# Kernel optimization log

Measured on AMD Instinct MI355X. Metric: run time of the kernel, lower is better.

Reference implementation:

```python
import jax, jax.numpy as jnp
import numpy as np

N, FIN, HID, HEADS, DHEAD = 4096, 512, 256, 4, 256
TOPK = 29  # hard-coded t=29 in HAN1.forward
FOUT = HEADS * DHEAD  # 1024


def setup_inputs() -> dict:
    key = jax.random.key(0)
    ks = jax.random.split(key, 12)
    h = jax.random.normal(ks[0], (N, FIN), dtype=jnp.float32)
    simlar = jax.random.normal(ks[1], (N, N), dtype=jnp.float32)
    # binary adjacency, avg degree ~41 so top-k (29) actually prunes
    adj = (jax.random.uniform(ks[2], (N, N)) < 0.01).astype(jnp.float32)
    s = 0.05
    W_trans = jax.random.normal(ks[3], (FIN, HID), dtype=jnp.float32) * s
    gat_W = jax.random.normal(ks[4], (HID, FOUT), dtype=jnp.float32) * s
    attn_l = jax.random.normal(ks[5], (HEADS, DHEAD), dtype=jnp.float32) * s
    attn_r = jax.random.normal(ks[6], (HEADS, DHEAD), dtype=jnp.float32) * s
    gat_bias = jnp.zeros((FOUT,), dtype=jnp.float32)
    sem_W1 = jax.random.normal(ks[7], (FOUT, 128), dtype=jnp.float32) * s
    sem_b1 = jnp.zeros((128,), dtype=jnp.float32)
    sem_W2 = jax.random.normal(ks[8], (128, 1), dtype=jnp.float32) * s
    return {"h": h, "simlar": simlar, "adj": adj, "W_trans": W_trans,
            "gat_W": gat_W, "attn_l": attn_l, "attn_r": attn_r,
            "gat_bias": gat_bias, "sem_W1": sem_W1, "sem_b1": sem_b1,
            "sem_W2": sem_W2}


def reference(h, simlar, adj, W_trans, gat_W, attn_l, attn_r, gat_bias,
              sem_W1, sem_b1, sem_W2):
    lrelu01 = lambda x: jax.nn.leaky_relu(x, 0.01)  # nn.LeakyReLU default
    # ---- adjacency sparsification: per-row top-k of filtered similarity ----
    filt = lrelu01(adj * simlar) * (adj > 0).astype(adj.dtype)  # [N,N]
    top_vals, top_idx = jax.lax.top_k(filt, TOPK)               # [N,TOPK]
    rows = jnp.arange(N)[:, None]
    newmat = jnp.zeros_like(filt).at[rows, top_idx].set(top_vals)
    mask = newmat != 0  # mask[src, dst]: edge src->dst (nonzero() semantics)
    # ---- feature transform (dropout p=0 -> identity) ----
    x = lrelu01(h @ W_trans)                                    # [N,HID]
    # ---- GATConv (DGL semantics, negative_slope=0.2, activation=elu) ----
    feat = (x @ gat_W).reshape(N, HEADS, DHEAD)                 # [N,H,D]
    el = jnp.einsum('nhd,hd->nh', feat, attn_l)                 # src scores
    er = jnp.einsum('nhd,hd->nh', feat, attn_r)                 # dst scores
    e = jax.nn.leaky_relu(el[:, None, :] + er[None, :, :], 0.2) # [src,dst,H]
    mask3 = mask[:, :, None]
    e = jnp.where(mask3, e, jnp.asarray(-1e30, e.dtype))
    emax = jnp.max(e, axis=0, keepdims=True)
    exp_e = jnp.where(mask3, jnp.exp(e - emax), 0.0)
    denom = jnp.sum(exp_e, axis=0, keepdims=True)
    alpha = exp_e / jnp.maximum(denom, 1e-20)  # zero-in-degree -> zero output
    rst = jnp.einsum('sdh,shf->dhf', alpha, feat)               # [N,H,D]
    rst = jax.nn.elu(rst + gat_bias.reshape(HEADS, DHEAD))
    sem = rst.reshape(N, FOUT)                                  # flatten(1)
    # ---- semantic attention over meta-paths (here: 1 meta-path) ----
    z = sem[:, None, :]                                         # [N,1,F]
    w = (jnp.tanh(z @ sem_W1 + sem_b1) @ sem_W2).mean(0)        # [1,1]
    beta = jax.nn.softmax(w, axis=0)                            # [1,1]
    out = (beta[None, :, :] * z).sum(1)                         # [N,F]
    return out
```

## Files before the change

kernel.cpp:

```cpp
#include <hip/hip_runtime.h>
#include <hip/hip_bf16.h>
#include <math.h>

#define N 4096
#define FIN 512
#define HID 256
#define HEADS 4
#define DHEAD 256
#define FOUT 1024
#define TOPK 29
#define CAP 64
#define CAPC 96

typedef __attribute__((ext_vector_type(8))) short short8;
typedef __attribute__((ext_vector_type(4))) float f32x4;
typedef __hip_bfloat16 bf16;

__device__ __forceinline__ float bflo(unsigned int u) {
  return __uint_as_float(u << 16);
}
__device__ __forceinline__ float bfhi(unsigned int u) {
  return __uint_as_float(u & 0xffff0000u);
}

__global__ __launch_bounds__(256) void scan_kernel(
    const float* __restrict__ h, const float* __restrict__ W_trans,
    const float* __restrict__ gat_W, const float* __restrict__ adj,
    const float* __restrict__ simlar, bf16* __restrict__ hb,
    bf16* __restrict__ Wtb, bf16* __restrict__ gWtb,
    int* __restrict__ colcnt, int* __restrict__ colsrc) {
  const int t = threadIdx.x;
  const int s = blockIdx.x;
  {
    const int H4 = N * FIN / 4;
    const int WT = HID * FIN;
    const int GT = FOUT * HID;
    const int total = H4 + WT + GT;
    const int stride = gridDim.x * 256;
    for (int i = s * 256 + t; i < total; i += stride) {
      if (i < H4) {
        const float4 v = reinterpret_cast<const float4*>(h)[i];
        bf16 tmp[4];
        tmp[0] = __float2bfloat16(v.x);
        tmp[1] = __float2bfloat16(v.y);
        tmp[2] = __float2bfloat16(v.z);
        tmp[3] = __float2bfloat16(v.w);
        *reinterpret_cast<ushort4*>(&hb[(size_t)i * 4]) =
            *reinterpret_cast<ushort4*>(tmp);
      } else if (i < H4 + WT) {
        const int j = i - H4;
        const int row = j >> 9, k = j & 511;
        Wtb[j] = __float2bfloat16(W_trans[(size_t)k * HID + row]);
      } else {
        const int j = i - H4 - WT;
        const int row = j >> 8, k = j & 255;
        gWtb[j] = __float2bfloat16(gat_W[(size_t)k * FOUT + row]);
      }
    }
  }
  __shared__ float swv[CAP];
  __shared__ int swi[CAP];
  __shared__ int cnt;
  if (t == 0) cnt = 0;
  __syncthreads();
  const float4* rowadj = reinterpret_cast<const float4*>(adj) + (size_t)s * (N / 4);
  const float4* rowsim = reinterpret_cast<const float4*>(simlar) + (size_t)s * (N / 4);
  float4 a[4];
#pragma unroll
  for (int it = 0; it < 4; ++it) a[it] = rowadj[it * 256 + t];
#pragma unroll
  for (int it = 0; it < 4; ++it) {
    const int j = it * 256 + t;
    if (a[it].x > 0.f || a[it].y > 0.f || a[it].z > 0.f || a[it].w > 0.f) {
      const float4 s4 = rowsim[j];
      const float aa[4] = {a[it].x, a[it].y, a[it].z, a[it].w};
      const float ss[4] = {s4.x, s4.y, s4.z, s4.w};
#pragma unroll
      for (int c = 0; c < 4; ++c) {
        if (aa[c] > 0.f && ss[c] > 0.f) {
          const int p = atomicAdd(&cnt, 1);
          if (p < CAP) {
            swv[p] = ss[c];
            swi[p] = j * 4 + c;
          }
        }
      }
    }
  }
  __syncthreads();
  const int C = min(cnt, CAP);
  if (t < C) {
    const float x = swv[t];
    int rk = 0;
    for (int jj = 0; jj < C; ++jj) rk += (swv[jj] > x);
    if (rk < TOPK) {
      const int d = swi[t];
      const int p = atomicAdd(&colcnt[d], 1);
      if (p < CAPC) colsrc[(size_t)d * CAPC + p] = s;
    }
  }
}

template <int OUTMODE>
__global__ __launch_bounds__(256) void gemm_mfma(const bf16* __restrict__ A,
                                                 const bf16* __restrict__ Bt,
                                                 bf16* __restrict__ Cb,
                                                 int M, int Nn, int K) {
  __shared__ bf16 As[64][72];
  __shared__ bf16 Bs[64][72];
  const int t = threadIdx.x;
  const int bm = blockIdx.x * 64, bn = blockIdx.y * 64;
  const int w = t >> 6, lane = t & 63, r = lane & 15, g = lane >> 4;
  const int m = t >> 2, c0 = (t & 3) * 8;
  f32x4 acc[4] = {};
  for (int k0 = 0; k0 < K; k0 += 64) {
    const bf16* arow = &A[(size_t)(bm + m) * K + k0];
    const bf16* brow = &Bt[(size_t)(bn + m) * K + k0];
    *reinterpret_cast<int4*>(&As[m][c0]) = *reinterpret_cast<const int4*>(&arow[c0]);
    *reinterpret_cast<int4*>(&As[m][c0 + 32]) = *reinterpret_cast<const int4*>(&arow[c0 + 32]);
    *reinterpret_cast<int4*>(&Bs[m][c0]) = *reinterpret_cast<const int4*>(&brow[c0]);
    *reinterpret_cast<int4*>(&Bs[m][c0 + 32]) = *reinterpret_cast<const int4*>(&brow[c0 + 32]);
    __syncthreads();
    const short8 a0 = *reinterpret_cast<short8*>(&As[w * 16 + r][g * 8]);
    const short8 a1 = *reinterpret_cast<short8*>(&As[w * 16 + r][32 + g * 8]);
#pragma unroll
    for (int j = 0; j < 4; ++j) {
      const short8 b0 = *reinterpret_cast<short8*>(&Bs[j * 16 + r][g * 8]);
      const short8 b1 = *reinterpret_cast<short8*>(&Bs[j * 16 + r][32 + g * 8]);
      acc[j] = __builtin_amdgcn_mfma_f32_16x16x32_bf16(a0, b0, acc[j], 0, 0, 0);
      acc[j] = __builtin_amdgcn_mfma_f32_16x16x32_bf16(a1, b1, acc[j], 0, 0, 0);
    }
    __syncthreads();
  }
#pragma unroll
  for (int j = 0; j < 4; ++j)
#pragma unroll
    for (int q = 0; q < 4; ++q) {
      const int row = bm + w * 16 + g * 4 + q;
      const int col = bn + j * 16 + r;
      float v = acc[j][q];
      if (OUTMODE == 1) v = v >= 0.f ? v : 0.01f * v;
      Cb[(size_t)row * Nn + col] = __float2bfloat16(v);
    }
}

__global__ __launch_bounds__(256) void elr_kernel(const bf16* __restrict__ featb,
                                                  const float* __restrict__ attn_l,
                                                  const float* __restrict__ attn_r,
                                                  float* __restrict__ el,
                                                  float* __restrict__ er) {
  const int n = blockIdx.x;
  const int h = threadIdx.x >> 6, lane = threadIdx.x & 63;
  const uint2 v2 = *reinterpret_cast<const uint2*>(
      &featb[(size_t)n * FOUT + h * DHEAD + lane * 4]);
  const float f0 = bflo(v2.x), f1 = bfhi(v2.x), f2 = bflo(v2.y), f3 = bfhi(v2.y);
  const float4 al = *reinterpret_cast<const float4*>(&attn_l[h * DHEAD + lane * 4]);
  const float4 ar = *reinterpret_cast<const float4*>(&attn_r[h * DHEAD + lane * 4]);
  float sl = f0 * al.x + f1 * al.y + f2 * al.z + f3 * al.w;
  float sr = f0 * ar.x + f1 * ar.y + f2 * ar.z + f3 * ar.w;
  for (int off = 32; off; off >>= 1) {
    sl += __shfl_xor(sl, off);
    sr += __shfl_xor(sr, off);
  }
  if (lane == 0) {
    el[n * HEADS + h] = sl;
    er[n * HEADS + h] = sr;
  }
}

__global__ __launch_bounds__(256) void agg_kernel(const int* __restrict__ colcnt,
                                                  const int* __restrict__ colsrc,
                                                  const float* __restrict__ el,
                                                  const float* __restrict__ er,
                                                  const bf16* __restrict__ featb,
                                                  const float* __restrict__ bias,
                                                  float* __restrict__ out) {
  __shared__ int tmp[2][CAPC];
  __shared__ int slist[2][CAPC];
  __shared__ float pbuf[2][HEADS][CAPC];
  const int t = threadIdx.x;
  const int grp = t >> 7;
  const int g = t & 127;
  const int d = blockIdx.x * 2 + grp;
  const int C = min(colcnt[d], CAPC);
  if (g < C) tmp[grp][g] = colsrc[(size_t)d * CAPC + g];
  __syncthreads();
  if (g < C) {
    const int v = tmp[grp][g];
    int rk = 0;
    for (int j = 0; j < C; ++j) rk += (tmp[grp][j] < v);
    slist[grp][rk] = v;
  }
  __syncthreads();
  const int h = g >> 5;
  const int hl = g & 31;
  const float er_dh = er[d * HEADS + h];
  float m = -INFINITY;
  for (int i = hl; i < C; i += 32) {
    float e = el[slist[grp][i] * HEADS + h] + er_dh;
    e = e >= 0.f ? e : 0.2f * e;
    pbuf[grp][h][i] = e;
    m = fmaxf(m, e);
  }
#pragma unroll
  for (int off = 16; off; off >>= 1) m = fmaxf(m, __shfl_xor(m, off));
  float dsum = 0.f;
  for (int i = hl; i < C; i += 32) {
    const float p = __expf(pbuf[grp][h][i] - m);
    pbuf[grp][h][i] = p;
    dsum += p;
  }
#pragma unroll
  for (int off = 16; off; off >>= 1) dsum += __shfl_xor(dsum, off);
  __syncthreads();
  float acc[8] = {};
  int i = 0;
  for (; i + 2 <= C; i += 2) {
    const float p0 = pbuf[grp][h][i];
    const float p1 = pbuf[grp][h][i + 1];
    const uint4 v0 = *reinterpret_cast<const uint4*>(
        &featb[(size_t)slist[grp][i] * FOUT + g * 8]);
    const uint4 v1 = *reinterpret_cast<const uint4*>(
        &featb[(size_t)slist[grp][i + 1] * FOUT + g * 8]);
    acc[0] = fmaf(p0, bflo(v0.x), acc[0]);
    acc[1] = fmaf(p0, bfhi(v0.x), acc[1]);
    acc[2] = fmaf(p0, bflo(v0.y), acc[2]);
    acc[3] = fmaf(p0, bfhi(v0.y), acc[3]);
    acc[4] = fmaf(p0, bflo(v0.z), acc[4]);
    acc[5] = fmaf(p0, bfhi(v0.z), acc[5]);
    acc[6] = fmaf(p0, bflo(v0.w), acc[6]);
    acc[7] = fmaf(p0, bfhi(v0.w), acc[7]);
    acc[0] = fmaf(p1, bflo(v1.x), acc[0]);
    acc[1] = fmaf(p1, bfhi(v1.x), acc[1]);
    acc[2] = fmaf(p1, bflo(v1.y), acc[2]);
    acc[3] = fmaf(p1, bfhi(v1.y), acc[3]);
    acc[4] = fmaf(p1, bflo(v1.z), acc[4]);
    acc[5] = fmaf(p1, bfhi(v1.z), acc[5]);
    acc[6] = fmaf(p1, bflo(v1.w), acc[6]);
    acc[7] = fmaf(p1, bfhi(v1.w), acc[7]);
  }
  if (i < C) {
    const float p0 = pbuf[grp][h][i];
    const uint4 v0 = *reinterpret_cast<const uint4*>(
        &featb[(size_t)slist[grp][i] * FOUT + g * 8]);
    acc[0] = fmaf(p0, bflo(v0.x), acc[0]);
    acc[1] = fmaf(p0, bfhi(v0.x), acc[1]);
    acc[2] = fmaf(p0, bflo(v0.y), acc[2]);
    acc[3] = fmaf(p0, bfhi(v0.y), acc[3]);
    acc[4] = fmaf(p0, bflo(v0.z), acc[4]);
    acc[5] = fmaf(p0, bfhi(v0.z), acc[5]);
    acc[6] = fmaf(p0, bflo(v0.w), acc[6]);
    acc[7] = fmaf(p0, bfhi(v0.w), acc[7]);
  }
  const float inv = C > 0 ? 1.f / dsum : 0.f;
  float o[8];
#pragma unroll
  for (int k = 0; k < 8; ++k) {
    const float r = acc[k] * inv + bias[g * 8 + k];
    o[k] = r > 0.f ? r : expm1f(r);
  }
  float* op = &out[(size_t)d * FOUT + g * 8];
  *reinterpret_cast<float4*>(op) = make_float4(o[0], o[1], o[2], o[3]);
  *reinterpret_cast<float4*>(op + 4) = make_float4(o[4], o[5], o[6], o[7]);
}

extern "C" void kernel_launch(void* const* d_in, const int* in_sizes, int n_in,
                              void* d_out, int out_size, void* d_ws, size_t ws_size,
                              hipStream_t stream) {
  const float* h        = (const float*)d_in[0];
  const float* simlar   = (const float*)d_in[1];
  const float* adj      = (const float*)d_in[2];
  const float* W_trans  = (const float*)d_in[3];
  const float* gat_W    = (const float*)d_in[4];
  const float* attn_l   = (const float*)d_in[5];
  const float* attn_r   = (const float*)d_in[6];
  const float* gat_bias = (const float*)d_in[7];
  float* out = (float*)d_out;

  char* ws = (char*)d_ws;
  const size_t MB = 1 << 20;
  bf16* hb    = (bf16*)(ws);
  bf16* Wtb   = (bf16*)(ws + 4 * MB);
  bf16* gWtb  = (bf16*)(ws + 4 * MB + 512 * 1024);
  bf16* xb    = (bf16*)(ws + 5 * MB);
  float* el   = (float*)(ws + 7 * MB);
  float* er   = (float*)(ws + 7 * MB + 65536);
  bf16* featb = (bf16*)(ws + 8 * MB);
  int* colcnt = (int*)(ws + 16 * MB);
  int* colsrc = (int*)(ws + 17 * MB);

  hipMemsetAsync(colcnt, 0, (size_t)N * sizeof(int), stream);
  scan_kernel<<<N, 256, 0, stream>>>(h, W_trans, gat_W, adj, simlar,
                                     hb, Wtb, gWtb, colcnt, colsrc);
  gemm_mfma<1><<<dim3(N / 64, HID / 64), 256, 0, stream>>>(hb, Wtb, xb, N, HID, FIN);
  gemm_mfma<2><<<dim3(N / 64, FOUT / 64), 256, 0, stream>>>(xb, gWtb, featb, N, FOUT, HID);
  elr_kernel<<<N, 256, 0, stream>>>(featb, attn_l, attn_r, el, er);
  agg_kernel<<<N / 2, 256, 0, stream>>>(colcnt, colsrc, el, er, featb, gat_bias, out);
}
```

Measured before the change: 75.59 us.

## Fold attention vectors into weights, add 128-tile GEMM, rebalance aggregation

Precomputes gat_W·attn_l and gat_W·attn_r inside the scan kernel, so el/er come straight from x with a small 256-wide dot product and no longer need to read featb. The feature GEMM moves to a new 128x128 tile kernel with larger per-wave accumulators to improve operand reuse. The aggregation kernel is reorganised so each block handles 4 destinations over half the feature width, one wave per destination. The el/er values now come from fp32 folded weights instead of bf16 feat, which slightly changes rounding, and the 128-tile GEMM launches only 256 blocks.

```diff
diff --git a/kernel.cpp b/kernel.cpp
--- a/kernel.cpp
+++ b/kernel.cpp
@@ -25,17 +25,20 @@
 
 __global__ __launch_bounds__(256) void scan_kernel(
     const float* __restrict__ h, const float* __restrict__ W_trans,
-    const float* __restrict__ gat_W, const float* __restrict__ adj,
+    const float* __restrict__ gat_W, const float* __restrict__ attn_l,
+    const float* __restrict__ attn_r, const float* __restrict__ adj,
     const float* __restrict__ simlar, bf16* __restrict__ hb,
     bf16* __restrict__ Wtb, bf16* __restrict__ gWtb,
-    int* __restrict__ colcnt, int* __restrict__ colsrc) {
+    float* __restrict__ alr2, int* __restrict__ colcnt,
+    int* __restrict__ colsrc) {
   const int t = threadIdx.x;
   const int s = blockIdx.x;
   {
     const int H4 = N * FIN / 4;
     const int WT = HID * FIN;
     const int GT = FOUT * HID;
-    const int total = H4 + WT + GT;
+    const int AL = 2 * HEADS * HID;
+    const int total = H4 + WT + GT + AL;
     const int stride = gridDim.x * 256;
     for (int i = s * 256 + t; i < total; i += stride) {
       if (i < H4) {
@@ -51,10 +54,20 @@
         const int j = i - H4;
         const int row = j >> 9, k = j & 511;
         Wtb[j] = __float2bfloat16(W_trans[(size_t)k * HID + row]);
-      } else {
+      } else if (i < H4 + WT + GT) {
         const int j = i - H4 - WT;
         const int row = j >> 8, k = j & 255;
         gWtb[j] = __float2bfloat16(gat_W[(size_t)k * FOUT + row]);
+      } else {
+        const int j = i - H4 - WT - GT;
+        const float* vec = (j < 1024) ? attn_l : attn_r;
+        const int jj = j & 1023;
+        const int hh = jj >> 8, k = jj & 255;
+        const float* wp = &gat_W[(size_t)k * FOUT + hh * DHEAD];
+        const float* vp = &vec[hh * DHEAD];
+        float acc = 0.f;
+        for (int d = 0; d < DHEAD; ++d) acc = fmaf(wp[d], vp[d], acc);
+        alr2[j] = acc;
       }
     }
   }
@@ -101,11 +114,10 @@
   }
 }
 
-template <int OUTMODE>
-__global__ __launch_bounds__(256) void gemm_mfma(const bf16* __restrict__ A,
-                                                 const bf16* __restrict__ Bt,
-                                                 bf16* __restrict__ Cb,
-                                                 int M, int Nn, int K) {
+__global__ __launch_bounds__(256) void gemm_mfma64(const bf16* __restrict__ A,
+                                                   const bf16* __restrict__ Bt,
+                                                   bf16* __restrict__ Cb,
+                                                   int M, int Nn, int K) {
   __shared__ bf16 As[64][72];
   __shared__ bf16 Bs[64][72];
   const int t = threadIdx.x;
@@ -139,32 +151,86 @@
       const int row = bm + w * 16 + g * 4 + q;
       const int col = bn + j * 16 + r;
       float v = acc[j][q];
-      if (OUTMODE == 1) v = v >= 0.f ? v : 0.01f * v;
+      v = v >= 0.f ? v : 0.01f * v;
       Cb[(size_t)row * Nn + col] = __float2bfloat16(v);
     }
 }
 
-__global__ __launch_bounds__(256) void elr_kernel(const bf16* __restrict__ featb,
-                                                  const float* __restrict__ attn_l,
-                                                  const float* __restrict__ attn_r,
-                                                  float* __restrict__ el,
-                                                  float* __restrict__ er) {
-  const int n = blockIdx.x;
-  const int h = threadIdx.x >> 6, lane = threadIdx.x & 63;
-  const uint2 v2 = *reinterpret_cast<const uint2*>(
-      &featb[(size_t)n * FOUT + h * DHEAD + lane * 4]);
-  const float f0 = bflo(v2.x), f1 = bfhi(v2.x), f2 = bflo(v2.y), f3 = bfhi(v2.y);
-  const float4 al = *reinterpret_cast<const float4*>(&attn_l[h * DHEAD + lane * 4]);
-  const float4 ar = *reinterpret_cast<const float4*>(&attn_r[h * DHEAD + lane * 4]);
-  float sl = f0 * al.x + f1 * al.y + f2 * al.z + f3 * al.w;
-  float sr = f0 * ar.x + f1 * ar.y + f2 * ar.z + f3 * ar.w;
+__global__ __launch_bounds__(256) void gemm_mfma128(const bf16* __restrict__ A,
+                                                    const bf16* __restrict__ Bt,
+                                                    bf16* __restrict__ Cb,
+                                                    int M, int Nn, int K) {
+  __shared__ bf16 As[128][40];
+  __shared__ bf16 Bs[128][40];
+  const int t = threadIdx.x;
+  const int bm = blockIdx.x * 128, bn = blockIdx.y * 128;
+  const int w = t >> 6, lane = t & 63, r = lane & 15, g = lane >> 4;
+  const int m = t >> 1, c0 = (t & 1) * 16;
+  f32x4 acc[2][8] = {};
+  for (int k0 = 0; k0 < K; k0 += 32) {
+    const bf16* arow = &A[(size_t)(bm + m) * K + k0 + c0];
+    const bf16* brow = &Bt[(size_t)(bn + m) * K + k0 + c0];
+    *reinterpret_cast<int4*>(&As[m][c0]) = *reinterpret_cast<const int4*>(arow);
+    *reinterpret_cast<int4*>(&As[m][c0 + 8]) = *reinterpret_cast<const int4*>(arow + 8);
+    *reinterpret_cast<int4*>(&Bs[m][c0]) = *reinterpret_cast<const int4*>(brow);
+    *reinterpret_cast<int4*>(&Bs[m][c0 + 8]) = *reinterpret_cast<const int4*>(brow + 8);
+    __syncthreads();
+    const short8 a0 = *reinterpret_cast<short8*>(&As[w * 32 + r][g * 8]);
+    const short8 a1 = *reinterpret_cast<short8*>(&As[w * 32 + 16 + r][g * 8]);
+#pragma unroll
+    for (int j = 0; j < 8; ++j) {
+      const short8 b = *reinterpret_cast<short8*>(&Bs[j * 16 + r][g * 8]);
+      acc[0][j] = __builtin_amdgcn_mfma_f32_16x16x32_bf16(a0, b, acc[0][j], 0, 0, 0);
+      acc[1][j] = __builtin_amdgcn_mfma_f32_16x16x32_bf16(a1, b, acc[1][j], 0, 0, 0);
+    }
+    __syncthreads();
+  }
+#pragma unroll
+  for (int i = 0; i < 2; ++i)
+#pragma unroll
+    for (int j = 0; j < 8; ++j)
+#pragma unroll
+      for (int q = 0; q < 4; ++q) {
+        const int row = bm + w * 32 + i * 16 + g * 4 + q;
+        const int col = bn + j * 16 + r;
+        Cb[(size_t)row * Nn + col] = __float2bfloat16(acc[i][j][q]);
+      }
+}
+
+__global__ __launch_bounds__(256) void elr2_kernel(const bf16* __restrict__ xb,
+                                                   const float* __restrict__ alr2,
+                                                   float* __restrict__ el,
+                                                   float* __restrict__ er) {
+  __shared__ float alrs[2048];
+  const int t = threadIdx.x;
+  for (int i = t; i < 2048; i += 256) alrs[i] = alr2[i];
+  __syncthreads();
+  const int wv = t >> 6, lane = t & 63;
+  const int n = blockIdx.x * 4 + wv;
+  const uint2 v2 = *reinterpret_cast<const uint2*>(&xb[(size_t)n * HID + lane * 4]);
+  const float xf[4] = {bflo(v2.x), bfhi(v2.x), bflo(v2.y), bfhi(v2.y)};
+  float pl[4], pr[4];
+#pragma unroll
+  for (int hh = 0; hh < 4; ++hh) {
+    const int base = hh * 256 + lane * 4;
+    pl[hh] = xf[0] * alrs[base] + xf[1] * alrs[base + 1] +
+             xf[2] * alrs[base + 2] + xf[3] * alrs[base + 3];
+    pr[hh] = xf[0] * alrs[1024 + base] + xf[1] * alrs[1024 + base + 1] +
+             xf[2] * alrs[1024 + base + 2] + xf[3] * alrs[1024 + base + 3];
+  }
   for (int off = 32; off; off >>= 1) {
-    sl += __shfl_xor(sl, off);
-    sr += __shfl_xor(sr, off);
+#pragma unroll
+    for (int hh = 0; hh < 4; ++hh) {
+      pl[hh] += __shfl_xor(pl[hh], off);
+      pr[hh] += __shfl_xor(pr[hh], off);
+    }
   }
   if (lane == 0) {
-    el[n * HEADS + h] = sl;
-    er[n * HEADS + h] = sr;
+#pragma unroll
+    for (int hh = 0; hh < 4; ++hh) {
+      el[n * HEADS + hh] = pl[hh];
+      er[n * HEADS + hh] = pr[hh];
+    }
   }
 }
 
@@ -175,53 +241,56 @@
                                                   const bf16* __restrict__ featb,
                                                   const float* __restrict__ bias,
                                                   float* __restrict__ out) {
-  __shared__ int tmp[2][CAPC];
-  __shared__ int slist[2][CAPC];
-  __shared__ float pbuf[2][HEADS][CAPC];
-  const int t = threadIdx.x;
-  const int grp = t >> 7;
-  const int g = t & 127;
-  const int d = blockIdx.x * 2 + grp;
+  __shared__ int tmp[4][CAPC];
+  __shared__ int slist[4][CAPC];
+  __shared__ float pbuf[4][2][CAPC];
+  const int t = threadIdx.x;
+  const int grp = t >> 6;
+  const int lane = t & 63;
+  const int hf = blockIdx.x & 1;
+  const int d = (blockIdx.x >> 1) * 4 + grp;
   const int C = min(colcnt[d], CAPC);
-  if (g < C) tmp[grp][g] = colsrc[(size_t)d * CAPC + g];
-  __syncthreads();
-  if (g < C) {
-    const int v = tmp[grp][g];
+  for (int i = lane; i < C; i += 64) tmp[grp][i] = colsrc[(size_t)d * CAPC + i];
+  __syncthreads();
+  for (int i = lane; i < C; i += 64) {
+    const int v = tmp[grp][i];
     int rk = 0;
     for (int j = 0; j < C; ++j) rk += (tmp[grp][j] < v);
     slist[grp][rk] = v;
   }
   __syncthreads();
-  const int h = g >> 5;
-  const int hl = g & 31;
+  const int sl = lane >> 5;
+  const int h = hf * 2 + sl;
+  const int hl = lane & 31;
   const float er_dh = er[d * HEADS + h];
   float m = -INFINITY;
   for (int i = hl; i < C; i += 32) {
     float e = el[slist[grp][i] * HEADS + h] + er_dh;
     e = e >= 0.f ? e : 0.2f * e;
-    pbuf[grp][h][i] = e;
+    pbuf[grp][sl][i] = e;
     m = fmaxf(m, e);
   }
 #pragma unroll
   for (int off = 16; off; off >>= 1) m = fmaxf(m, __shfl_xor(m, off));
   float dsum = 0.f;
   for (int i = hl; i < C; i += 32) {
-    const float p = __expf(pbuf[grp][h][i] - m);
-    pbuf[grp][h][i] = p;
+    const float p = __expf(pbuf[grp][sl][i] - m);
+    pbuf[grp][sl][i] = p;
     dsum += p;
   }
 #pragma unroll
   for (int off = 16; off; off >>= 1) dsum += __shfl_xor(dsum, off);
   __syncthreads();
+  const size_t dimoff = hf * 512 + lane * 8;
   float acc[8] = {};
   int i = 0;
   for (; i + 2 <= C; i += 2) {
-    const float p0 = pbuf[grp][h][i];
-    const float p1 = pbuf[grp][h][i + 1];
+    const float p0 = pbuf[grp][sl][i];
+    const float p1 = pbuf[grp][sl][i + 1];
     const uint4 v0 = *reinterpret_cast<const uint4*>(
-        &featb[(size_t)slist[grp][i] * FOUT + g * 8]);
+        &featb[(size_t)slist[grp][i] * FOUT + dimoff]);
     const uint4 v1 = *reinterpret_cast<const uint4*>(
-        &featb[(size_t)slist[grp][i + 1] * FOUT + g * 8]);
+        &featb[(size_t)slist[grp][i + 1] * FOUT + dimoff]);
     acc[0] = fmaf(p0, bflo(v0.x), acc[0]);
     acc[1] = fmaf(p0, bfhi(v0.x), acc[1]);
     acc[2] = fmaf(p0, bflo(v0.y), acc[2]);
@@ -240,9 +309,9 @@
     acc[7] = fmaf(p1, bfhi(v1.w), acc[7]);
   }
   if (i < C) {
-    const float p0 = pbuf[grp][h][i];
+    const float p0 = pbuf[grp][sl][i];
     const uint4 v0 = *reinterpret_cast<const uint4*>(
-        &featb[(size_t)slist[grp][i] * FOUT + g * 8]);
+        &featb[(size_t)slist[grp][i] * FOUT + dimoff]);
     acc[0] = fmaf(p0, bflo(v0.x), acc[0]);
     acc[1] = fmaf(p0, bfhi(v0.x), acc[1]);
     acc[2] = fmaf(p0, bflo(v0.y), acc[2]);
@@ -256,10 +325,10 @@
   float o[8];
 #pragma unroll
   for (int k = 0; k < 8; ++k) {
-    const float r = acc[k] * inv + bias[g * 8 + k];
+    const float r = acc[k] * inv + bias[dimoff + k];
     o[k] = r > 0.f ? r : expm1f(r);
   }
-  float* op = &out[(size_t)d * FOUT + g * 8];
+  float* op = &out[(size_t)d * FOUT + dimoff];
   *reinterpret_cast<float4*>(op) = make_float4(o[0], o[1], o[2], o[3]);
   *reinterpret_cast<float4*>(op + 4) = make_float4(o[4], o[5], o[6], o[7]);
 }
@@ -285,15 +354,16 @@
   bf16* xb    = (bf16*)(ws + 5 * MB);
   float* el   = (float*)(ws + 7 * MB);
   float* er   = (float*)(ws + 7 * MB + 65536);
+  float* alr2 = (float*)(ws + 7 * MB + 131072);
   bf16* featb = (bf16*)(ws + 8 * MB);
   int* colcnt = (int*)(ws + 16 * MB);
   int* colsrc = (int*)(ws + 17 * MB);
 
   hipMemsetAsync(colcnt, 0, (size_t)N * sizeof(int), stream);
-  scan_kernel<<<N, 256, 0, stream>>>(h, W_trans, gat_W, adj, simlar,
-                                     hb, Wtb, gWtb, colcnt, colsrc);
-  gemm_mfma<1><<<dim3(N / 64, HID / 64), 256, 0, stream>>>(hb, Wtb, xb, N, HID, FIN);
-  gemm_mfma<2><<<dim3(N / 64, FOUT / 64), 256, 0, stream>>>(xb, gWtb, featb, N, FOUT, HID);
-  elr_kernel<<<N, 256, 0, stream>>>(featb, attn_l, attn_r, el, er);
+  scan_kernel<<<N, 256, 0, stream>>>(h, W_trans, gat_W, attn_l, attn_r, adj,
+                                     simlar, hb, Wtb, gWtb, alr2, colcnt, colsrc);
+  gemm_mfma64<<<dim3(N / 64, HID / 64), 256, 0, stream>>>(hb, Wtb, xb, N, HID, FIN);
+  gemm_mfma128<<<dim3(N / 128, FOUT / 128), 256, 0, stream>>>(xb, gWtb, featb, N, FOUT, HID);
+  elr2_kernel<<<N / 4, 256, 0, stream>>>(xb, alr2, el, er);
   agg_kernel<<<N / 2, 256, 0, stream>>>(colcnt, colsrc, el, er, featb, gat_bias, out);
 }
```

After: 84.74 us. +12.1%, slower.
